# Performance work log

Measured on AMD Instinct MI355X. Metric: run time of the kernel, lower is better.

Reference implementation:

```python
import jax, jax.numpy as jnp
import numpy as np

MARGIN = 0.5
AP_VALUE = 0.8
AN_VALUE = 0.4
ABS_W = 1.0


def setup_inputs() -> dict:
    key = jax.random.key(0)
    k1, k2 = jax.random.split(key)
    bs, d = 16384, 64
    inputs = jax.random.normal(k1, (bs, d), dtype=jnp.float32)
    target = jax.random.randint(k2, (bs,), 0, 64, dtype=jnp.int64)
    return {"inputs": inputs, "target": target}


def reference(inputs, target):
    # L2-normalize features (normalize_feature=True)
    x = inputs / jnp.linalg.norm(inputs, axis=-1, keepdims=True)

    # cross-entropy on normalized features treated as logits
    logp = jax.nn.log_softmax(x, axis=-1)  # [bs, d]
    loss_ce = -jnp.mean(jnp.take_along_axis(logp, target[:, None], axis=1))

    # cosine-similarity matrix [bs, bs]
    dist = x @ x.T

    is_pos = target[None, :] == target[:, None]
    # hard mining: min similarity among positives, max among negatives (per row)
    dist_ap = jnp.min(jnp.where(is_pos, dist, jnp.inf), axis=1)   # [bs]
    dist_an = jnp.max(jnp.where(is_pos, -jnp.inf, dist), axis=1)  # [bs]

    loss = jnp.mean(jax.nn.relu(MARGIN + dist_ap - dist_an))

    # absolute (angular margin) terms
    abs_ap = jax.nn.relu(AP_VALUE - dist_ap)
    abs_an = jax.nn.relu(dist_an - AN_VALUE)
    loss = (jnp.mean(abs_an) + jnp.mean(abs_ap)) * ABS_W + loss

    return loss + loss_ce
```

## Files before the change

kernel.cpp:

```cpp
#include <hip/hip_runtime.h>


#define N_ROWS 16384
#define N_DIM 64

typedef __attribute__((ext_vector_type(8))) short bf16x8;
typedef __attribute__((ext_vector_type(4))) float f32x4;

__device__ inline unsigned short f2bf(float f) {
  unsigned u = __float_as_uint(f);
  unsigned r = u + 0x7fffu + ((u >> 16) & 1u);
  return (unsigned short)(r >> 16);
}

__device__ inline unsigned enc_key(float f) {
  unsigned u = __float_as_uint(f);
  return (u & 0x80000000u) ? ~u : (u | 0x80000000u);
}
__device__ inline float dec_key(unsigned k) {
  unsigned u = (k & 0x80000000u) ? (k ^ 0x80000000u) : ~k;
  return __uint_as_float(u);
}

__device__ inline void g2lds16(const void* g, void* l) {
  __builtin_amdgcn_global_load_lds(
      (const __attribute__((address_space(1))) void*)g,
      (__attribute__((address_space(3))) void*)l, 16, 0, 0);
}

__global__ void prep_kernel(const float* __restrict__ x, const int* __restrict__ tgt,
                            unsigned short* __restrict__ xb, float* __restrict__ ce_row,
                            unsigned* __restrict__ mp_key, unsigned* __restrict__ mn_key,
                            float* __restrict__ out) {
  const int row  = blockIdx.x * 4 + (threadIdx.x >> 6);
  const int lane = threadIdx.x & 63;
  float v  = x[row * N_DIM + lane];
  float ss = v * v;
#pragma unroll
  for (int s = 1; s < 64; s <<= 1) ss += __shfl_xor(ss, s, 64);
  float xn = v * rsqrtf(ss);
  xb[row * N_DIM + lane] = f2bf(xn);

  float mx = xn;
#pragma unroll
  for (int s = 1; s < 64; s <<= 1) mx = fmaxf(mx, __shfl_xor(mx, s, 64));
  float e  = __expf(xn - mx);
  float se = e;
#pragma unroll
  for (int s = 1; s < 64; s <<= 1) se += __shfl_xor(se, s, 64);
  float lse = mx + __logf(se);
  int   t   = tgt[row];
  float xt  = __shfl(xn, t, 64);
  if (lane == 0) {
    ce_row[row] = lse - xt;
    mp_key[row] = 0xFFFFFFFFu;
    mn_key[row] = 0u;
  }
  if (blockIdx.x == 0 && threadIdx.x == 0) out[0] = 0.f;
}

__global__ __launch_bounds__(256, 8)
void mine_kernel(const unsigned short* __restrict__ xb, const int* __restrict__ tgt,
                 unsigned* __restrict__ mp_key, unsigned* __restrict__ mn_key) {
  __shared__ unsigned short Bt[2][4][1024];
  __shared__ unsigned short tjl[N_ROWS / 16];

  const int lane    = threadIdx.x & 63;
  const int wv      = threadIdx.x >> 6;
  const int iblk    = blockIdx.x >> 4;
  const int jspl    = blockIdx.x & 15;
  const int rowbase = iblk * 128 + wv * 32;
  const int m = lane & 15, q = lane >> 4;
  const int jbase = jspl * (N_ROWS / 16);

  bf16x8 a[2][2];
#pragma unroll
  for (int tr = 0; tr < 2; ++tr) {
    const unsigned short* p = xb + (rowbase + tr * 16 + m) * N_DIM + q * 8;
    a[tr][0] = *(const bf16x8*)(p);
    a[tr][1] = *(const bf16x8*)(p + 32);
  }
  int ti[2][4];
#pragma unroll
  for (int tr = 0; tr < 2; ++tr)
#pragma unroll
    for (int r = 0; r < 4; ++r)
      ti[tr][r] = tgt[rowbase + tr * 16 + q * 4 + r];

  float mp[8], mn[8];
#pragma unroll
  for (int k = 0; k < 8; ++k) { mp[k] = __builtin_inff(); mn[k] = -__builtin_inff(); }

  for (int k = threadIdx.x; k < N_ROWS / 16; k += 256)
    tjl[k] = (unsigned short)tgt[jbase + k];

  const unsigned short* src0 =
      xb + (jbase + (lane >> 3)) * N_DIM + (((lane & 7) ^ ((lane >> 3) & 7)) * 8);

  {
    const unsigned short* s = src0 + (wv * 16) * N_DIM;
    g2lds16(s,             (unsigned short*)&Bt[0][wv][0] + lane * 8);
    g2lds16(s + 8 * N_DIM, (unsigned short*)&Bt[0][wv][0] + 512 + lane * 8);
  }
  __syncthreads();

  const int roff0 = m * 128 + ((q * 16) ^ ((m & 7) << 4));
  const int roff1 = m * 128 + (((64) + q * 16) ^ ((m & 7) << 4));

  for (int ph = 0; ph < 16; ++ph) {
    const int pb = ph & 1;
    if (ph < 15) {
      const unsigned short* s = src0 + ((ph + 1) * 64 + wv * 16) * N_DIM;
      g2lds16(s,             (unsigned short*)&Bt[pb ^ 1][wv][0] + lane * 8);
      g2lds16(s + 8 * N_DIM, (unsigned short*)&Bt[pb ^ 1][wv][0] + 512 + lane * 8);
    }
#pragma unroll 1
    for (int j4 = 0; j4 < 4; ++j4) {
      const int jc = ph * 4 + j4;
      const char* bb = (const char*)&Bt[pb][j4][0];
      const bf16x8 cb0 = *(const bf16x8*)(bb + roff0);
      const bf16x8 cb1 = *(const bf16x8*)(bb + roff1);
      const int    ctj = tjl[jc * 16 + m];

#pragma unroll
      for (int tr = 0; tr < 2; ++tr) {
        f32x4 acc = {0.f, 0.f, 0.f, 0.f};
        acc = __builtin_amdgcn_mfma_f32_16x16x32_bf16(a[tr][0], cb0, acc, 0, 0, 0);
        acc = __builtin_amdgcn_mfma_f32_16x16x32_bf16(a[tr][1], cb1, acc, 0, 0, 0);
#pragma unroll
        for (int r = 0; r < 4; ++r) {
          const bool  pos = (ctj == ti[tr][r]);
          const float d   = acc[r];
          const int   k   = tr * 4 + r;
          mp[k] = fminf(mp[k], pos ? d : __builtin_inff());
          mn[k] = fmaxf(mn[k], pos ? -__builtin_inff() : d);
        }
      }
    }
    __syncthreads();
  }

#pragma unroll
  for (int s = 1; s < 16; s <<= 1) {
#pragma unroll
    for (int k = 0; k < 8; ++k) {
      mp[k] = fminf(mp[k], __shfl_xor(mp[k], s, 64));
      mn[k] = fmaxf(mn[k], __shfl_xor(mn[k], s, 64));
    }
  }
  if (m == 0) {
#pragma unroll
    for (int tr = 0; tr < 2; ++tr)
#pragma unroll
      for (int r = 0; r < 4; ++r) {
        const int row = rowbase + tr * 16 + q * 4 + r;
        atomicMin(&mp_key[row], enc_key(mp[tr * 4 + r]));
        atomicMax(&mn_key[row], enc_key(mn[tr * 4 + r]));
      }
  }
}

__global__ void finalize_kernel(const unsigned* __restrict__ mp_key, const unsigned* __restrict__ mn_key,
                                const float* __restrict__ ce_row, float* __restrict__ out) {
  __shared__ float red[16];
  float s = 0.f;
#pragma unroll
  for (int it = 0; it < 2; ++it) {
    const int r = it * 8192 + blockIdx.x * 1024 + threadIdx.x;
    float ap = dec_key(mp_key[r]);
    float an = dec_key(mn_key[r]);
    s += fmaxf(0.5f + ap - an, 0.f) + fmaxf(0.8f - ap, 0.f) +
         fmaxf(an - 0.4f, 0.f) + ce_row[r];
  }
#pragma unroll
  for (int sh = 1; sh < 64; sh <<= 1) s += __shfl_xor(s, sh, 64);
  const int wv = threadIdx.x >> 6;
  if ((threadIdx.x & 63) == 0) red[wv] = s;
  __syncthreads();
  if (threadIdx.x == 0) {
    float t = 0.f;
#pragma unroll
    for (int w = 0; w < 16; ++w) t += red[w];
    atomicAdd(out, t * (1.0f / N_ROWS));
  }
}

extern "C" void kernel_launch(void* const* d_in, const int* in_sizes, int n_in,
                              void* d_out, int out_size, void* d_ws, size_t ws_size,
                              hipStream_t stream) {
  const float* x   = (const float*)d_in[0];
  const int*   tgt = (const int*)d_in[1];
  char* ws = (char*)d_ws;

  unsigned short* xb     = (unsigned short*)ws;
  unsigned*       mp_key = (unsigned*)(ws + (2u << 20));
  unsigned*       mn_key = (unsigned*)(ws + (2u << 20) + (64u << 10));
  float*          ce_row = (float*)(ws + (2u << 20) + (128u << 10));
  float*          out    = (float*)d_out;

  prep_kernel<<<N_ROWS / 4, 256, 0, stream>>>(x, tgt, xb, ce_row, mp_key, mn_key, out);
  mine_kernel<<<(N_ROWS / 128) * 16, 256, 0, stream>>>(xb, tgt, mp_key, mn_key);
  finalize_kernel<<<8, 1024, 0, stream>>>(mp_key, mn_key, ce_row, out);
}
```

Before: 156.4 us.

## Sort rows by class so mining tiles skip per-element label compares

Adds a histogram, a serial scan and a scatter pass that reorder the bf16 features and labels by class. The mining kernel then checks whether a 16-column tile's label range overlaps the 32-row group's range. Tiles with no overlap take a negatives-only max path, tiles where all labels match take a positives-only min path, and only mixed tiles do the per-element masked compare. Labels are also packed into bytes to save registers. In exchange it adds extra launches, a memset, a single-threaded scan, and a scatter copy of the features.

```diff
diff --git a/kernel.cpp b/kernel.cpp
--- a/kernel.cpp
+++ b/kernel.cpp
@@ -3,8 +3,10 @@
 
 #define N_ROWS 16384
 #define N_DIM 64
+#define N_CLS 64
 
 typedef __attribute__((ext_vector_type(8))) short bf16x8;
+typedef __attribute__((ext_vector_type(8))) unsigned short ushort8;
 typedef __attribute__((ext_vector_type(4))) float f32x4;
 
 __device__ inline unsigned short f2bf(float f) {
@@ -31,7 +33,7 @@
 __global__ void prep_kernel(const float* __restrict__ x, const int* __restrict__ tgt,
                             unsigned short* __restrict__ xb, float* __restrict__ ce_row,
                             unsigned* __restrict__ mp_key, unsigned* __restrict__ mn_key,
-                            float* __restrict__ out) {
+                            unsigned* __restrict__ hist, float* __restrict__ out) {
   const int row  = blockIdx.x * 4 + (threadIdx.x >> 6);
   const int lane = threadIdx.x & 63;
   float v  = x[row * N_DIM + lane];
@@ -55,12 +57,34 @@
     ce_row[row] = lse - xt;
     mp_key[row] = 0xFFFFFFFFu;
     mn_key[row] = 0u;
+    atomicAdd(&hist[t], 1u);
   }
   if (blockIdx.x == 0 && threadIdx.x == 0) out[0] = 0.f;
 }
 
+__global__ void scan_kernel(const unsigned* __restrict__ hist, unsigned* __restrict__ cursor) {
+  if (threadIdx.x == 0) {
+    unsigned run = 0;
+    for (int c = 0; c < N_CLS; ++c) { cursor[c] = run; run += hist[c]; }
+  }
+}
+
+__global__ void scatter_kernel(const unsigned short* __restrict__ xb, const int* __restrict__ tgt,
+                               unsigned* __restrict__ cursor, unsigned short* __restrict__ xbs,
+                               unsigned short* __restrict__ tgs) {
+  const int lane = threadIdx.x & 63;
+  const int sub  = lane & 7;
+  const int row  = blockIdx.x * 32 + (threadIdx.x >> 6) * 8 + (lane >> 3);
+  const int c    = tgt[row];
+  int dst = 0;
+  if (sub == 0) dst = (int)atomicAdd(&cursor[c], 1u);
+  dst = __shfl(dst, lane & 56, 64);
+  ((ushort8*)xbs)[dst * 8 + sub] = ((const ushort8*)xb)[row * 8 + sub];
+  if (sub == 0) tgs[dst] = (unsigned short)c;
+}
+
 __global__ __launch_bounds__(256, 8)
-void mine_kernel(const unsigned short* __restrict__ xb, const int* __restrict__ tgt,
+void mine_kernel(const unsigned short* __restrict__ xbs, const unsigned short* __restrict__ tgs,
                  unsigned* __restrict__ mp_key, unsigned* __restrict__ mn_key) {
   __shared__ unsigned short Bt[2][4][1024];
   __shared__ unsigned short tjl[N_ROWS / 16];
@@ -76,26 +100,30 @@
   bf16x8 a[2][2];
 #pragma unroll
   for (int tr = 0; tr < 2; ++tr) {
-    const unsigned short* p = xb + (rowbase + tr * 16 + m) * N_DIM + q * 8;
+    const unsigned short* p = xbs + (rowbase + tr * 16 + m) * N_DIM + q * 8;
     a[tr][0] = *(const bf16x8*)(p);
     a[tr][1] = *(const bf16x8*)(p + 32);
   }
-  int ti[2][4];
-#pragma unroll
-  for (int tr = 0; tr < 2; ++tr)
+  unsigned tip[2];
+#pragma unroll
+  for (int tr = 0; tr < 2; ++tr) {
+    unsigned vv = 0;
 #pragma unroll
     for (int r = 0; r < 4; ++r)
-      ti[tr][r] = tgt[rowbase + tr * 16 + q * 4 + r];
+      vv |= ((unsigned)tgs[rowbase + tr * 16 + q * 4 + r] & 0xffu) << (8 * r);
+    tip[tr] = vv;
+  }
+  const int clo = __builtin_amdgcn_readfirstlane((int)tgs[rowbase]);
+  const int chi = __builtin_amdgcn_readfirstlane((int)tgs[rowbase + 31]);
 
   float mp[8], mn[8];
 #pragma unroll
   for (int k = 0; k < 8; ++k) { mp[k] = __builtin_inff(); mn[k] = -__builtin_inff(); }
 
-  for (int k = threadIdx.x; k < N_ROWS / 16; k += 256)
-    tjl[k] = (unsigned short)tgt[jbase + k];
+  for (int k = threadIdx.x; k < N_ROWS / 16; k += 256) tjl[k] = tgs[jbase + k];
 
   const unsigned short* src0 =
-      xb + (jbase + (lane >> 3)) * N_DIM + (((lane & 7) ^ ((lane >> 3) & 7)) * 8);
+      xbs + (jbase + (lane >> 3)) * N_DIM + (((lane & 7) ^ ((lane >> 3) & 7)) * 8);
 
   {
     const unsigned short* s = src0 + (wv * 16) * N_DIM;
@@ -120,20 +148,40 @@
       const char* bb = (const char*)&Bt[pb][j4][0];
       const bf16x8 cb0 = *(const bf16x8*)(bb + roff0);
       const bf16x8 cb1 = *(const bf16x8*)(bb + roff1);
-      const int    ctj = tjl[jc * 16 + m];
-
-#pragma unroll
-      for (int tr = 0; tr < 2; ++tr) {
-        f32x4 acc = {0.f, 0.f, 0.f, 0.f};
-        acc = __builtin_amdgcn_mfma_f32_16x16x32_bf16(a[tr][0], cb0, acc, 0, 0, 0);
-        acc = __builtin_amdgcn_mfma_f32_16x16x32_bf16(a[tr][1], cb1, acc, 0, 0, 0);
+      const int tlo = __builtin_amdgcn_readfirstlane((int)tjl[jc * 16]);
+      const int thi = __builtin_amdgcn_readfirstlane((int)tjl[jc * 16 + 15]);
+
+      f32x4 acc0 = {0.f, 0.f, 0.f, 0.f}, acc1 = {0.f, 0.f, 0.f, 0.f};
+      acc0 = __builtin_amdgcn_mfma_f32_16x16x32_bf16(a[0][0], cb0, acc0, 0, 0, 0);
+      acc0 = __builtin_amdgcn_mfma_f32_16x16x32_bf16(a[0][1], cb1, acc0, 0, 0, 0);
+      acc1 = __builtin_amdgcn_mfma_f32_16x16x32_bf16(a[1][0], cb0, acc1, 0, 0, 0);
+      acc1 = __builtin_amdgcn_mfma_f32_16x16x32_bf16(a[1][1], cb1, acc1, 0, 0, 0);
+
+      if (thi < clo || tlo > chi) {
 #pragma unroll
         for (int r = 0; r < 4; ++r) {
-          const bool  pos = (ctj == ti[tr][r]);
-          const float d   = acc[r];
-          const int   k   = tr * 4 + r;
-          mp[k] = fminf(mp[k], pos ? d : __builtin_inff());
-          mn[k] = fmaxf(mn[k], pos ? -__builtin_inff() : d);
+          mn[r]     = fmaxf(mn[r],     acc0[r]);
+          mn[4 + r] = fmaxf(mn[4 + r], acc1[r]);
+        }
+      } else if (clo == chi && tlo == thi && tlo == clo) {
+#pragma unroll
+        for (int r = 0; r < 4; ++r) {
+          mp[r]     = fminf(mp[r],     acc0[r]);
+          mp[4 + r] = fminf(mp[4 + r], acc1[r]);
+        }
+      } else {
+        const unsigned ctj = (unsigned)tjl[jc * 16 + m] & 0xffu;
+#pragma unroll
+        for (int tr = 0; tr < 2; ++tr) {
+          const f32x4 ac = tr ? acc1 : acc0;
+#pragma unroll
+          for (int r = 0; r < 4; ++r) {
+            const bool  pos = (((tip[tr] >> (8 * r)) & 0xffu) == ctj);
+            const float d   = ac[r];
+            const int   k   = tr * 4 + r;
+            mp[k] = fminf(mp[k], pos ? d : __builtin_inff());
+            mn[k] = fmaxf(mn[k], pos ? -__builtin_inff() : d);
+          }
         }
       }
     }
@@ -193,12 +241,19 @@
   char* ws = (char*)d_ws;
 
   unsigned short* xb     = (unsigned short*)ws;
-  unsigned*       mp_key = (unsigned*)(ws + (2u << 20));
-  unsigned*       mn_key = (unsigned*)(ws + (2u << 20) + (64u << 10));
-  float*          ce_row = (float*)(ws + (2u << 20) + (128u << 10));
+  unsigned short* xbs    = (unsigned short*)(ws + (2u << 20));
+  unsigned*       mp_key = (unsigned*)(ws + (4u << 20));
+  unsigned*       mn_key = (unsigned*)(ws + (4u << 20) + (64u << 10));
+  float*          ce_row = (float*)(ws + (4u << 20) + (128u << 10));
+  unsigned short* tgs    = (unsigned short*)(ws + (4u << 20) + (192u << 10));
+  unsigned*       hist   = (unsigned*)(ws + (4u << 20) + (224u << 10));
+  unsigned*       cursor = hist + 64;
   float*          out    = (float*)d_out;
 
-  prep_kernel<<<N_ROWS / 4, 256, 0, stream>>>(x, tgt, xb, ce_row, mp_key, mn_key, out);
-  mine_kernel<<<(N_ROWS / 128) * 16, 256, 0, stream>>>(xb, tgt, mp_key, mn_key);
+  hipMemsetAsync(hist, 0, 256, stream);
+  prep_kernel<<<N_ROWS / 4, 256, 0, stream>>>(x, tgt, xb, ce_row, mp_key, mn_key, hist, out);
+  scan_kernel<<<1, 64, 0, stream>>>(hist, cursor);
+  scatter_kernel<<<N_ROWS / 32, 256, 0, stream>>>(xb, tgt, cursor, xbs, tgs);
+  mine_kernel<<<(N_ROWS / 128) * 16, 256, 0, stream>>>(xbs, tgs, mp_key, mn_key);
   finalize_kernel<<<8, 1024, 0, stream>>>(mp_key, mn_key, ce_row, out);
 }
```

Measured after the change: 270.8 us. 73.1% more time.
